# Performance work log

Hardware: AMD Instinct MI355X
Metric: run time of the kernel (lower is better)

The kernel has to match this reference:

```python
import jax, jax.numpy as jnp
import numpy as np

N_NODES = 100000
N_HEDGES = 20000
N_PAIRS = 1600000
D = 128


def setup_inputs() -> dict:
    key = jax.random.key(0)
    k1, k2, k3, k4, k5 = jax.random.split(key, 5)
    features = jax.random.normal(k1, (N_NODES, D), dtype=jnp.float32)
    W = jax.random.normal(k2, (D, D), dtype=jnp.float32) * (1.0 / np.sqrt(D))
    b = jax.random.normal(k3, (D,), dtype=jnp.float32) * 0.01
    node_idx = jax.random.randint(k4, (N_PAIRS,), 0, N_NODES, dtype=jnp.int32)
    hedge_idx = jax.random.randint(k5, (N_PAIRS,), 0, N_HEDGES, dtype=jnp.int32)
    return {"features": features, "W": W, "b": b,
            "node_idx": node_idx, "hedge_idx": hedge_idx, "n_hedges": N_HEDGES}


def reference(features, W, b, node_idx, hedge_idx, n_hedges):
    # features: [N, D]; (node_idx, hedge_idx): [E] incidence pairs
    N = features.shape[0]
    ones = jnp.ones(node_idx.shape, dtype=features.dtype)
    # node -> hyperedge mean (DGL copy_u + mean over 'in' etype)
    deg_e = jax.ops.segment_sum(ones, hedge_idx, num_segments=n_hedges)  # [He]
    h_edge = jax.ops.segment_sum(features[node_idx], hedge_idx, num_segments=n_hedges)
    h_edge = h_edge / jnp.maximum(deg_e, 1.0)[:, None]  # zero-degree edges -> 0
    # hyperedge -> node mean (copy_u + mean over 'contains' etype)
    deg_n = jax.ops.segment_sum(ones, node_idx, num_segments=N)  # [N]
    h_node = jax.ops.segment_sum(h_edge[hedge_idx], node_idx, num_segments=N)
    h_node = h_node / jnp.maximum(deg_n, 1.0)[:, None]
    # nn.Linear: x @ W.T + b
    return h_node @ W.T + b
```

## Files before the change

### kernel.cpp

```cpp
#include <hip/hip_runtime.h>

static constexpr int kD = 128;
static constexpr int kHedges = 20000;

static constexpr int kNCE = 157;
static constexpr int kCapCE = 11264;
static constexpr int kNCN = 196;
static constexpr int kCapCN = 9216;
static constexpr int kSliceE = 896;
static constexpr int kSliceN = 768;
static constexpr int kPmax = 3200;

__device__ __forceinline__ float u2f(unsigned u) { return __uint_as_float(u); }
__device__ __forceinline__ unsigned f2u(float f) { return __float_as_uint(f); }

__device__ __forceinline__ unsigned bfpack(float x, float y) {
  unsigned ux = f2u(x); ux = (ux + 0x7FFFu + ((ux >> 16) & 1u)) >> 16;
  unsigned uy = f2u(y); uy = (uy + 0x7FFFu + ((uy >> 16) & 1u)) & 0xFFFF0000u;
  return ux | uy;
}
__device__ __forceinline__ void bf8_acc(uint4 v, float* a) {
  a[0] += u2f(v.x << 16); a[1] += u2f(v.x & 0xFFFF0000u);
  a[2] += u2f(v.y << 16); a[3] += u2f(v.y & 0xFFFF0000u);
  a[4] += u2f(v.z << 16); a[5] += u2f(v.z & 0xFFFF0000u);
  a[6] += u2f(v.w << 16); a[7] += u2f(v.w & 0xFFFF0000u);
}

__global__ __launch_bounds__(256) void partition_coarse(
    const float* __restrict__ feat, unsigned* __restrict__ feat_bf, int n_feat,
    const int* __restrict__ node_idx, const int* __restrict__ hedge_idx,
    int n_pairs,
    int* __restrict__ gcnt_e, int* __restrict__ buf_e,
    int* __restrict__ gcnt_n, int* __restrict__ buf_n) {
  __shared__ unsigned lbuf_e[kPmax];
  __shared__ unsigned lbuf_n[kPmax];
  __shared__ int he[kNCE], se[kNCE];
  __shared__ int hn[kNCN], sn_[kNCN];
  __shared__ int wtot[4];
  const int tid = threadIdx.x;
  {
    const int n8 = n_feat >> 3;
    for (int t = blockIdx.x * 256 + tid; t < n8; t += gridDim.x * 256) {
      long long i = (long long)t * 8;
      const float4 v0 = *(const float4*)(feat + i);
      const float4 v1 = *(const float4*)(feat + i + 4);
      uint4 o;
      o.x = bfpack(v0.x, v0.y); o.y = bfpack(v0.z, v0.w);
      o.z = bfpack(v1.x, v1.y); o.w = bfpack(v1.z, v1.w);
      *(uint4*)(feat_bf + (i >> 1)) = o;
    }
  }
  const int per_block = (n_pairs + gridDim.x - 1) / gridDim.x;
  const int s = blockIdx.x * per_block;
  const int e = min(s + per_block, n_pairs);
  const int cnt = max(e - s, 0);
  for (int i = tid; i < kNCE; i += 256) he[i] = 0;
  for (int i = tid; i < kNCN; i += 256) hn[i] = 0;
  __syncthreads();
  for (int i = s + tid; i < e; i += 256) {
    atomicAdd(&he[hedge_idx[i] >> 7], 1);
    atomicAdd(&hn[node_idx[i] >> 9], 1);
  }
  __syncthreads();
  const int lane = tid & 63, wid = tid >> 6;
  {
    int v = (tid < kNCE) ? he[tid] : 0;
    int x = v;
#pragma unroll
    for (int d = 1; d < 64; d <<= 1) {
      int y = __shfl_up(x, d, 64);
      if (lane >= d) x += y;
    }
    if (lane == 63) wtot[wid] = x;
    __syncthreads();
    int add = 0;
    for (int w = 0; w < wid; ++w) add += wtot[w];
    if (tid < kNCE) {
      int lofs = x + add - v;
      int base = (v > 0) ? atomicAdd(&gcnt_e[tid], v) : 0;
      se[tid] = base - lofs;
      he[tid] = lofs;
    }
  }
  __syncthreads();
  {
    int v = (tid < kNCN) ? hn[tid] : 0;
    int x = v;
#pragma unroll
    for (int d = 1; d < 64; d <<= 1) {
      int y = __shfl_up(x, d, 64);
      if (lane >= d) x += y;
    }
    if (lane == 63) wtot[wid] = x;
    __syncthreads();
    int add = 0;
    for (int w = 0; w < wid; ++w) add += wtot[w];
    if (tid < kNCN) {
      int lofs = x + add - v;
      int base = (v > 0) ? atomicAdd(&gcnt_n[tid], v) : 0;
      sn_[tid] = base - lofs;
      hn[tid] = lofs;
    }
  }
  __syncthreads();
  for (int i = s + tid; i < e; i += 256) {
    const unsigned n = (unsigned)node_idx[i];
    const unsigned h = (unsigned)hedge_idx[i];
    const int be = (int)(h >> 7);
    const int p = atomicAdd(&he[be], 1);
    lbuf_e[p] = (n << 15) | h;
    const int bn = (int)(n >> 9);
    const int q = atomicAdd(&hn[bn], 1);
    lbuf_n[q] = (h << 17) | n;
  }
  __syncthreads();
  for (int i = tid; i < cnt; i += 256) {
    const unsigned v = lbuf_e[i];
    const int h = (int)(v & 0x7FFFu);
    const int n = (int)(v >> 15);
    const int b = h >> 7;
    const int pe = se[b] + i;
    if (pe < kCapCE) buf_e[(long long)b * kCapCE + pe] = (n << 7) | (h & 127);
  }
  for (int i = tid; i < cnt; i += 256) {
    const unsigned v = lbuf_n[i];
    const int n = (int)(v & 0x1FFFFu);
    const int h = (int)(v >> 17);
    const int b = n >> 9;
    const int pn = sn_[b] + i;
    if (pn < kCapCN) buf_n[(long long)b * kCapCN + pn] = (h << 9) | (n & 511);
  }
}

__global__ __launch_bounds__(512) void subsort_kernel(
    int* __restrict__ buf_e, const int* __restrict__ gcnt_e, int* __restrict__ seg_e,
    int* __restrict__ buf_n, const int* __restrict__ gcnt_n, int* __restrict__ seg_n) {
  __shared__ int sbuf[kCapCE];
  __shared__ int bins[513];
  __shared__ int cur[512];
  __shared__ int segs[513];
  __shared__ int wtot[8];
  const int tid = threadIdx.x;
  int nbins, shift, cnt; int* src; int* segout;
  if (blockIdx.x < kNCE) {
    int cb = blockIdx.x; nbins = 128; shift = 7;
    src = buf_e + (long long)cb * kCapCE;
    cnt = min(gcnt_e[cb], kCapCE);
    segout = seg_e + cb * 129;
  } else {
    int cb = blockIdx.x - kNCE; nbins = 512; shift = 9;
    src = buf_n + (long long)cb * kCapCN;
    cnt = min(gcnt_n[cb], kCapCN);
    segout = seg_n + cb * 513;
  }
  const int mask = nbins - 1;
  for (int i = tid; i < nbins; i += 512) bins[i] = 0;
  __syncthreads();
  for (int i = tid; i < cnt; i += 512) atomicAdd(&bins[src[i] & mask], 1);
  __syncthreads();
  const int lane = tid & 63, wid = tid >> 6;
  int v = (tid < nbins) ? bins[tid] : 0;
  int x = v;
#pragma unroll
  for (int d = 1; d < 64; d <<= 1) {
    int y = __shfl_up(x, d, 64);
    if (lane >= d) x += y;
  }
  if (lane == 63) wtot[wid] = x;
  __syncthreads();
  int add = 0;
  for (int w = 0; w < wid; ++w) add += wtot[w];
  if (tid < nbins) { segs[tid + 1] = x + add; cur[tid] = x + add - v; }
  if (tid == 0) segs[0] = 0;
  __syncthreads();
  for (int i = tid; i < cnt; i += 512) {
    int p = src[i];
    int r = atomicAdd(&cur[p & mask], 1);
    sbuf[r] = p >> shift;
  }
  __syncthreads();
  for (int i = tid; i < cnt; i += 512) src[i] = sbuf[i];
  for (int j = tid; j <= nbins; j += 512) segout[j] = segs[j];
}

__global__ __launch_bounds__(128) void gather_edge_v2(
    const unsigned* __restrict__ feat_bf, const int* __restrict__ buf_e,
    const int* __restrict__ seg_e, unsigned* __restrict__ h_edge, int n_hedges) {
  __shared__ int ebuf[kSliceE];
  __shared__ int segl[9];
  const int b = blockIdx.x;
  const int tid = threadIdx.x;
  const int h0 = b * 8;
  const int cb = h0 >> 7, j0 = h0 & 127;
  if (tid < 9) segl[tid] = seg_e[cb * 129 + j0 + tid];
  __syncthreads();
  const int sbase = segl[0];
  const int n_sl = min(segl[8] - sbase, kSliceE);
  const int* src = buf_e + (long long)cb * kCapCE + sbase;
  for (int i = tid; i < n_sl; i += 128) ebuf[i] = src[i];
  __syncthreads();
  const int g = tid >> 4, lane = tid & 15, cw = lane * 4;
  int gh = h0 + g;
  if (gh >= n_hedges) return;
  const int deg = segl[g + 1] - segl[g];
  const int s0 = min(segl[g] - sbase, n_sl);
  const int e0 = min(segl[g + 1] - sbase, n_sl);
  float a[8] = {}, a2[8] = {};
  int j = s0;
  for (; j + 7 < e0; j += 8) {
    uint4 v0 = *(const uint4*)(feat_bf + (long long)ebuf[j] * 64 + cw);
    uint4 v1 = *(const uint4*)(feat_bf + (long long)ebuf[j + 1] * 64 + cw);
    uint4 v2 = *(const uint4*)(feat_bf + (long long)ebuf[j + 2] * 64 + cw);
    uint4 v3 = *(const uint4*)(feat_bf + (long long)ebuf[j + 3] * 64 + cw);
    uint4 v4 = *(const uint4*)(feat_bf + (long long)ebuf[j + 4] * 64 + cw);
    uint4 v5 = *(const uint4*)(feat_bf + (long long)ebuf[j + 5] * 64 + cw);
    uint4 v6 = *(const uint4*)(feat_bf + (long long)ebuf[j + 6] * 64 + cw);
    uint4 v7 = *(const uint4*)(feat_bf + (long long)ebuf[j + 7] * 64 + cw);
    bf8_acc(v0, a); bf8_acc(v1, a2); bf8_acc(v2, a); bf8_acc(v3, a2);
    bf8_acc(v4, a); bf8_acc(v5, a2); bf8_acc(v6, a); bf8_acc(v7, a2);
  }
  for (; j < e0; ++j) {
    uint4 v = *(const uint4*)(feat_bf + (long long)ebuf[j] * 64 + cw);
    bf8_acc(v, a);
  }
#pragma unroll
  for (int t = 0; t < 8; ++t) a[t] += a2[t];
  float inv = 1.0f / fmaxf((float)deg, 1.0f);
  uint4 o;
  o.x = bfpack(a[0] * inv, a[1] * inv);
  o.y = bfpack(a[2] * inv, a[3] * inv);
  o.z = bfpack(a[4] * inv, a[5] * inv);
  o.w = bfpack(a[6] * inv, a[7] * inv);
  *(uint4*)(h_edge + (long long)gh * 64 + cw) = o;
}

static constexpr int kWRow = 68;
__global__ __launch_bounds__(256) void edge_linear_v4(
    unsigned* __restrict__ h_edge, const float* __restrict__ W, int n_rows) {
  __shared__ unsigned Wt2[kD * kWRow];
  __shared__ float hT[kD * 64];
  const int tid = threadIdx.x;
  const int row0 = blockIdx.x * 64;
  for (int i = tid; i < kD * 64; i += 256) {
    int k = i & 127, j = i >> 7;
    float c0 = W[(2 * j) * kD + k];
    float c1 = W[(2 * j + 1) * kD + k];
    Wt2[k * kWRow + j] = bfpack(c0, c1);
  }
  {
    const int r = tid & 63, o = tid >> 6;
    const uint4* hp = (const uint4*)(h_edge + (long long)(row0 + r) * 64 + o * 16);
#pragma unroll
    for (int q = 0; q < 4; ++q) {
      uint4 v = hp[q];
      int k0 = o * 32 + q * 8;
      hT[(k0 + 0) * 64 + r] = u2f(v.x << 16);
      hT[(k0 + 1) * 64 + r] = u2f(v.x & 0xFFFF0000u);
      hT[(k0 + 2) * 64 + r] = u2f(v.y << 16);
      hT[(k0 + 3) * 64 + r] = u2f(v.y & 0xFFFF0000u);
      hT[(k0 + 4) * 64 + r] = u2f(v.z << 16);
      hT[(k0 + 5) * 64 + r] = u2f(v.z & 0xFFFF0000u);
      hT[(k0 + 6) * 64 + r] = u2f(v.w << 16);
      hT[(k0 + 7) * 64 + r] = u2f(v.w & 0xFFFF0000u);
    }
  }
  __syncthreads();
  const int c8 = tid & 15;
  const int rg = tid >> 4;
  float4 acc[4][2] = {};
#pragma unroll 2
  for (int k = 0; k < kD; ++k) {
    const uint4 wp = *(const uint4*)(&Wt2[k * kWRow + c8 * 4]);
    const float4 h4 = *(const float4*)(&hT[k * 64 + rg * 4]);
    const float w0 = u2f(wp.x << 16), w1 = u2f(wp.x & 0xFFFF0000u);
    const float w2 = u2f(wp.y << 16), w3 = u2f(wp.y & 0xFFFF0000u);
    const float w4 = u2f(wp.z << 16), w5 = u2f(wp.z & 0xFFFF0000u);
    const float w6 = u2f(wp.w << 16), w7 = u2f(wp.w & 0xFFFF0000u);
    const float hh[4] = {h4.x, h4.y, h4.z, h4.w};
#pragma unroll
    for (int i = 0; i < 4; ++i) {
      acc[i][0].x = fmaf(hh[i], w0, acc[i][0].x);
      acc[i][0].y = fmaf(hh[i], w1, acc[i][0].y);
      acc[i][0].z = fmaf(hh[i], w2, acc[i][0].z);
      acc[i][0].w = fmaf(hh[i], w3, acc[i][0].w);
      acc[i][1].x = fmaf(hh[i], w4, acc[i][1].x);
      acc[i][1].y = fmaf(hh[i], w5, acc[i][1].y);
      acc[i][1].z = fmaf(hh[i], w6, acc[i][1].z);
      acc[i][1].w = fmaf(hh[i], w7, acc[i][1].w);
    }
  }
  long long rr = row0 + rg * 4;
#pragma unroll
  for (int i = 0; i < 4; ++i) {
    uint4 o;
    o.x = bfpack(acc[i][0].x, acc[i][0].y);
    o.y = bfpack(acc[i][0].z, acc[i][0].w);
    o.z = bfpack(acc[i][1].x, acc[i][1].y);
    o.w = bfpack(acc[i][1].z, acc[i][1].w);
    *(uint4*)(h_edge + (rr + i) * 64 + c8 * 4) = o;
  }
}

__global__ __launch_bounds__(128) void gather_node_v2(
    const unsigned* __restrict__ t_edge, const int* __restrict__ buf_n,
    const int* __restrict__ seg_n, const float* __restrict__ bias,
    float* __restrict__ out, int n_nodes) {
  __shared__ int ebuf[kSliceN];
  __shared__ int segl[33];
  const int b = blockIdx.x;
  const int tid = threadIdx.x;
  const int n0 = b * 32;
  const int cb = n0 >> 9, j0 = n0 & 511;
  if (tid < 33) segl[tid] = seg_n[cb * 513 + j0 + tid];
  __syncthreads();
  const int sbase = segl[0];
  const int n_sl = min(segl[32] - sbase, kSliceN);
  const int* src = buf_n + (long long)cb * kCapCN + sbase;
  for (int i = tid; i < n_sl; i += 128) ebuf[i] = src[i];
  __syncthreads();
  const int g = tid >> 4, lane = tid & 15, cw = lane * 4;
  const float4 b0 = *(const float4*)(bias + lane * 8);
  const float4 b1 = *(const float4*)(bias + lane * 8 + 4);
  for (int nl = g; nl < 32; nl += 8) {
    int gn = n0 + nl;
    if (gn >= n_nodes) continue;
    const int deg = segl[nl + 1] - segl[nl];
    const int s0 = min(segl[nl] - sbase, n_sl);
    const int e0 = min(segl[nl + 1] - sbase, n_sl);
    float a[8] = {}, a2[8] = {};
    int j = s0;
    for (; j + 7 < e0; j += 8) {
      uint4 v0 = *(const uint4*)(t_edge + (long long)ebuf[j] * 64 + cw);
      uint4 v1 = *(const uint4*)(t_edge + (long long)ebuf[j + 1] * 64 + cw);
      uint4 v2 = *(const uint4*)(t_edge + (long long)ebuf[j + 2] * 64 + cw);
      uint4 v3 = *(const uint4*)(t_edge + (long long)ebuf[j + 3] * 64 + cw);
      uint4 v4 = *(const uint4*)(t_edge + (long long)ebuf[j + 4] * 64 + cw);
      uint4 v5 = *(const uint4*)(t_edge + (long long)ebuf[j + 5] * 64 + cw);
      uint4 v6 = *(const uint4*)(t_edge + (long long)ebuf[j + 6] * 64 + cw);
      uint4 v7 = *(const uint4*)(t_edge + (long long)ebuf[j + 7] * 64 + cw);
      bf8_acc(v0, a); bf8_acc(v1, a2); bf8_acc(v2, a); bf8_acc(v3, a2);
      bf8_acc(v4, a); bf8_acc(v5, a2); bf8_acc(v6, a); bf8_acc(v7, a2);
    }
    for (; j < e0; ++j) {
      uint4 v = *(const uint4*)(t_edge + (long long)ebuf[j] * 64 + cw);
      bf8_acc(v, a);
    }
#pragma unroll
    for (int t = 0; t < 8; ++t) a[t] += a2[t];
    float inv = 1.0f / fmaxf((float)deg, 1.0f);
    float4 o0, o1;
    o0.x = fmaf(a[0], inv, b0.x); o0.y = fmaf(a[1], inv, b0.y);
    o0.z = fmaf(a[2], inv, b0.z); o0.w = fmaf(a[3], inv, b0.w);
    o1.x = fmaf(a[4], inv, b1.x); o1.y = fmaf(a[5], inv, b1.y);
    o1.z = fmaf(a[6], inv, b1.z); o1.w = fmaf(a[7], inv, b1.w);
    float* op = out + (long long)gn * kD + lane * 8;
    *(float4*)op = o0;
    *(float4*)(op + 4) = o1;
  }
}

extern "C" void kernel_launch(void* const* d_in, const int* in_sizes, int n_in,
                              void* d_out, int out_size, void* d_ws, size_t ws_size,
                              hipStream_t stream) {
  const float* feat      = (const float*)d_in[0];
  const float* W         = (const float*)d_in[1];
  const float* b         = (const float*)d_in[2];
  const int*   node_idx  = (const int*)d_in[3];
  const int*   hedge_idx = (const int*)d_in[4];

  const int n_pairs  = in_sizes[3];
  const int n_nodes  = in_sizes[0] / kD;
  const int n_hedges = kHedges;
  const int n_feat   = in_sizes[0];

  unsigned* feat_bf = (unsigned*)d_out;

  const int n_rows_pad = ((n_hedges + 63) / 64) * 64;
  unsigned* h_edge = (unsigned*)d_ws;
  int* buf_e = (int*)(h_edge + (size_t)n_rows_pad * 64);
  int* buf_n = buf_e + (size_t)kNCE * kCapCE;
  int* seg_e = buf_n + (size_t)kNCN * kCapCN;
  int* seg_n = seg_e + (size_t)kNCE * 129;
  int* gcnt_e = seg_n + (size_t)kNCN * 513;
  int* gcnt_n = gcnt_e + kNCE;

  hipMemsetAsync(gcnt_e, 0, (size_t)(kNCE + kNCN) * sizeof(int), stream);

  int pgrid = (n_pairs + kPmax - 1) / kPmax;
  if (pgrid < 512) pgrid = 512;

  partition_coarse<<<pgrid, 256, 0, stream>>>(
      feat, feat_bf, n_feat,
      node_idx, hedge_idx, n_pairs, gcnt_e, buf_e, gcnt_n, buf_n);

  subsort_kernel<<<kNCE + kNCN, 512, 0, stream>>>(
      buf_e, gcnt_e, seg_e, buf_n, gcnt_n, seg_n);

  gather_edge_v2<<<(n_hedges + 7) / 8, 128, 0, stream>>>(
      feat_bf, buf_e, seg_e, h_edge, n_hedges);

  edge_linear_v4<<<n_rows_pad / 64, 256, 0, stream>>>(h_edge, W, n_rows_pad);

  gather_node_v2<<<(n_nodes + 31) / 32, 128, 0, stream>>>(
      h_edge, buf_n, seg_n, b, (float*)d_out, n_nodes);
}
```

Measured before the change: 277.2 us.

## Split gather kernels across eight feature-column slices per block group

Both gather kernels now launch eight blocks per node/hyperedge group, each block handling a 16-column slice with one 4-byte bf16-pair load per thread instead of a 16-byte load. This raises parallelism and occupancy, with 256-thread blocks and more hyperedges per block. The cost is that every slice block reloads the index list into shared memory, and the gathered loads are narrower and less coalesced. The edge slice buffer grows to 3072 entries, and the index loads and edge output stores become nontemporal.

```diff
diff --git a/kernel.cpp b/kernel.cpp
--- a/kernel.cpp
+++ b/kernel.cpp
@@ -7,7 +7,7 @@
 static constexpr int kCapCE = 11264;
 static constexpr int kNCN = 196;
 static constexpr int kCapCN = 9216;
-static constexpr int kSliceE = 896;
+static constexpr int kSliceE3 = 3072;
 static constexpr int kSliceN = 768;
 static constexpr int kPmax = 3200;
 
@@ -18,12 +18,6 @@
   unsigned ux = f2u(x); ux = (ux + 0x7FFFu + ((ux >> 16) & 1u)) >> 16;
   unsigned uy = f2u(y); uy = (uy + 0x7FFFu + ((uy >> 16) & 1u)) & 0xFFFF0000u;
   return ux | uy;
-}
-__device__ __forceinline__ void bf8_acc(uint4 v, float* a) {
-  a[0] += u2f(v.x << 16); a[1] += u2f(v.x & 0xFFFF0000u);
-  a[2] += u2f(v.y << 16); a[3] += u2f(v.y & 0xFFFF0000u);
-  a[4] += u2f(v.z << 16); a[5] += u2f(v.z & 0xFFFF0000u);
-  a[6] += u2f(v.w << 16); a[7] += u2f(v.w & 0xFFFF0000u);
 }
 
 __global__ __launch_bounds__(256) void partition_coarse(
@@ -183,55 +177,60 @@
   for (int j = tid; j <= nbins; j += 512) segout[j] = segs[j];
 }
 
-__global__ __launch_bounds__(128) void gather_edge_v2(
+__global__ __launch_bounds__(256) void gather_edge_v3(
     const unsigned* __restrict__ feat_bf, const int* __restrict__ buf_e,
     const int* __restrict__ seg_e, unsigned* __restrict__ h_edge, int n_hedges) {
-  __shared__ int ebuf[kSliceE];
-  __shared__ int segl[9];
-  const int b = blockIdx.x;
-  const int tid = threadIdx.x;
-  const int h0 = b * 8;
+  __shared__ int ebuf[kSliceE3];
+  __shared__ int segl[33];
+  const int bid = blockIdx.x;
+  const int slice = bid & 7;
+  const int hb = bid >> 3;
+  const int tid = threadIdx.x;
+  const int h0 = hb * 32;
   const int cb = h0 >> 7, j0 = h0 & 127;
-  if (tid < 9) segl[tid] = seg_e[cb * 129 + j0 + tid];
+  if (tid < 33) segl[tid] = seg_e[cb * 129 + j0 + tid];
   __syncthreads();
   const int sbase = segl[0];
-  const int n_sl = min(segl[8] - sbase, kSliceE);
+  const int n_sl = min(segl[32] - sbase, kSliceE3);
   const int* src = buf_e + (long long)cb * kCapCE + sbase;
-  for (int i = tid; i < n_sl; i += 128) ebuf[i] = src[i];
-  __syncthreads();
-  const int g = tid >> 4, lane = tid & 15, cw = lane * 4;
-  int gh = h0 + g;
+  for (int i = tid; i < n_sl; i += 256) ebuf[i] = __builtin_nontemporal_load(&src[i]);
+  __syncthreads();
+  const int g = tid >> 3, lane = tid & 7;
+  const int gh = h0 + g;
   if (gh >= n_hedges) return;
+  const int w = slice * 8 + lane;
+  const unsigned* fw = feat_bf + w;
   const int deg = segl[g + 1] - segl[g];
   const int s0 = min(segl[g] - sbase, n_sl);
   const int e0 = min(segl[g + 1] - sbase, n_sl);
-  float a[8] = {}, a2[8] = {};
+  float a0 = 0.f, a1 = 0.f, c0 = 0.f, c1 = 0.f;
   int j = s0;
   for (; j + 7 < e0; j += 8) {
-    uint4 v0 = *(const uint4*)(feat_bf + (long long)ebuf[j] * 64 + cw);
-    uint4 v1 = *(const uint4*)(feat_bf + (long long)ebuf[j + 1] * 64 + cw);
-    uint4 v2 = *(const uint4*)(feat_bf + (long long)ebuf[j + 2] * 64 + cw);
-    uint4 v3 = *(const uint4*)(feat_bf + (long long)ebuf[j + 3] * 64 + cw);
-    uint4 v4 = *(const uint4*)(feat_bf + (long long)ebuf[j + 4] * 64 + cw);
-    uint4 v5 = *(const uint4*)(feat_bf + (long long)ebuf[j + 5] * 64 + cw);
-    uint4 v6 = *(const uint4*)(feat_bf + (long long)ebuf[j + 6] * 64 + cw);
-    uint4 v7 = *(const uint4*)(feat_bf + (long long)ebuf[j + 7] * 64 + cw);
-    bf8_acc(v0, a); bf8_acc(v1, a2); bf8_acc(v2, a); bf8_acc(v3, a2);
-    bf8_acc(v4, a); bf8_acc(v5, a2); bf8_acc(v6, a); bf8_acc(v7, a2);
+    unsigned u0 = fw[(unsigned)ebuf[j] * 64u];
+    unsigned u1 = fw[(unsigned)ebuf[j + 1] * 64u];
+    unsigned u2 = fw[(unsigned)ebuf[j + 2] * 64u];
+    unsigned u3 = fw[(unsigned)ebuf[j + 3] * 64u];
+    unsigned u4 = fw[(unsigned)ebuf[j + 4] * 64u];
+    unsigned u5 = fw[(unsigned)ebuf[j + 5] * 64u];
+    unsigned u6 = fw[(unsigned)ebuf[j + 6] * 64u];
+    unsigned u7 = fw[(unsigned)ebuf[j + 7] * 64u];
+    a0 += u2f(u0 << 16); a1 += u2f(u0 & 0xFFFF0000u);
+    c0 += u2f(u1 << 16); c1 += u2f(u1 & 0xFFFF0000u);
+    a0 += u2f(u2 << 16); a1 += u2f(u2 & 0xFFFF0000u);
+    c0 += u2f(u3 << 16); c1 += u2f(u3 & 0xFFFF0000u);
+    a0 += u2f(u4 << 16); a1 += u2f(u4 & 0xFFFF0000u);
+    c0 += u2f(u5 << 16); c1 += u2f(u5 & 0xFFFF0000u);
+    a0 += u2f(u6 << 16); a1 += u2f(u6 & 0xFFFF0000u);
+    c0 += u2f(u7 << 16); c1 += u2f(u7 & 0xFFFF0000u);
   }
   for (; j < e0; ++j) {
-    uint4 v = *(const uint4*)(feat_bf + (long long)ebuf[j] * 64 + cw);
-    bf8_acc(v, a);
-  }
-#pragma unroll
-  for (int t = 0; t < 8; ++t) a[t] += a2[t];
-  float inv = 1.0f / fmaxf((float)deg, 1.0f);
-  uint4 o;
-  o.x = bfpack(a[0] * inv, a[1] * inv);
-  o.y = bfpack(a[2] * inv, a[3] * inv);
-  o.z = bfpack(a[4] * inv, a[5] * inv);
-  o.w = bfpack(a[6] * inv, a[7] * inv);
-  *(uint4*)(h_edge + (long long)gh * 64 + cw) = o;
+    unsigned u = fw[(unsigned)ebuf[j] * 64u];
+    a0 += u2f(u << 16); a1 += u2f(u & 0xFFFF0000u);
+  }
+  a0 += c0; a1 += c1;
+  const float inv = 1.0f / fmaxf((float)deg, 1.0f);
+  __builtin_nontemporal_store(bfpack(a0 * inv, a1 * inv),
+                              &h_edge[(unsigned)gh * 64u + w]);
 }
 
 static constexpr int kWRow = 68;
@@ -301,62 +300,56 @@
   }
 }
 
-__global__ __launch_bounds__(128) void gather_node_v2(
+__global__ __launch_bounds__(256) void gather_node_v3(
     const unsigned* __restrict__ t_edge, const int* __restrict__ buf_n,
     const int* __restrict__ seg_n, const float* __restrict__ bias,
     float* __restrict__ out, int n_nodes) {
   __shared__ int ebuf[kSliceN];
   __shared__ int segl[33];
-  const int b = blockIdx.x;
-  const int tid = threadIdx.x;
-  const int n0 = b * 32;
+  const int bid = blockIdx.x;
+  const int slice = bid & 7;
+  const int nb = bid >> 3;
+  const int tid = threadIdx.x;
+  const int n0 = nb * 32;
   const int cb = n0 >> 9, j0 = n0 & 511;
   if (tid < 33) segl[tid] = seg_n[cb * 513 + j0 + tid];
   __syncthreads();
   const int sbase = segl[0];
   const int n_sl = min(segl[32] - sbase, kSliceN);
   const int* src = buf_n + (long long)cb * kCapCN + sbase;
-  for (int i = tid; i < n_sl; i += 128) ebuf[i] = src[i];
-  __syncthreads();
-  const int g = tid >> 4, lane = tid & 15, cw = lane * 4;
-  const float4 b0 = *(const float4*)(bias + lane * 8);
-  const float4 b1 = *(const float4*)(bias + lane * 8 + 4);
-  for (int nl = g; nl < 32; nl += 8) {
-    int gn = n0 + nl;
-    if (gn >= n_nodes) continue;
-    const int deg = segl[nl + 1] - segl[nl];
-    const int s0 = min(segl[nl] - sbase, n_sl);
-    const int e0 = min(segl[nl + 1] - sbase, n_sl);
-    float a[8] = {}, a2[8] = {};
-    int j = s0;
-    for (; j + 7 < e0; j += 8) {
-      uint4 v0 = *(const uint4*)(t_edge + (long long)ebuf[j] * 64 + cw);
-      uint4 v1 = *(const uint4*)(t_edge + (long long)ebuf[j + 1] * 64 + cw);
-      uint4 v2 = *(const uint4*)(t_edge + (long long)ebuf[j + 2] * 64 + cw);
-      uint4 v3 = *(const uint4*)(t_edge + (long long)ebuf[j + 3] * 64 + cw);
-      uint4 v4 = *(const uint4*)(t_edge + (long long)ebuf[j + 4] * 64 + cw);
-      uint4 v5 = *(const uint4*)(t_edge + (long long)ebuf[j + 5] * 64 + cw);
-      uint4 v6 = *(const uint4*)(t_edge + (long long)ebuf[j + 6] * 64 + cw);
-      uint4 v7 = *(const uint4*)(t_edge + (long long)ebuf[j + 7] * 64 + cw);
-      bf8_acc(v0, a); bf8_acc(v1, a2); bf8_acc(v2, a); bf8_acc(v3, a2);
-      bf8_acc(v4, a); bf8_acc(v5, a2); bf8_acc(v6, a); bf8_acc(v7, a2);
-    }
-    for (; j < e0; ++j) {
-      uint4 v = *(const uint4*)(t_edge + (long long)ebuf[j] * 64 + cw);
-      bf8_acc(v, a);
-    }
-#pragma unroll
-    for (int t = 0; t < 8; ++t) a[t] += a2[t];
-    float inv = 1.0f / fmaxf((float)deg, 1.0f);
-    float4 o0, o1;
-    o0.x = fmaf(a[0], inv, b0.x); o0.y = fmaf(a[1], inv, b0.y);
-    o0.z = fmaf(a[2], inv, b0.z); o0.w = fmaf(a[3], inv, b0.w);
-    o1.x = fmaf(a[4], inv, b1.x); o1.y = fmaf(a[5], inv, b1.y);
-    o1.z = fmaf(a[6], inv, b1.z); o1.w = fmaf(a[7], inv, b1.w);
-    float* op = out + (long long)gn * kD + lane * 8;
-    *(float4*)op = o0;
-    *(float4*)(op + 4) = o1;
-  }
+  for (int i = tid; i < n_sl; i += 256) ebuf[i] = __builtin_nontemporal_load(&src[i]);
+  __syncthreads();
+  const int g = tid >> 3, lane = tid & 7;
+  const int gn = n0 + g;
+  if (gn >= n_nodes) return;
+  const int w = slice * 8 + lane;
+  const unsigned* tw = t_edge + w;
+  const float2 bb = *(const float2*)(bias + 2 * w);
+  const int deg = segl[g + 1] - segl[g];
+  const int s0 = min(segl[g] - sbase, n_sl);
+  const int e0 = min(segl[g + 1] - sbase, n_sl);
+  float a0 = 0.f, a1 = 0.f, c0 = 0.f, c1 = 0.f;
+  int j = s0;
+  for (; j + 3 < e0; j += 4) {
+    unsigned u0 = tw[(unsigned)ebuf[j] * 64u];
+    unsigned u1 = tw[(unsigned)ebuf[j + 1] * 64u];
+    unsigned u2 = tw[(unsigned)ebuf[j + 2] * 64u];
+    unsigned u3 = tw[(unsigned)ebuf[j + 3] * 64u];
+    a0 += u2f(u0 << 16); a1 += u2f(u0 & 0xFFFF0000u);
+    c0 += u2f(u1 << 16); c1 += u2f(u1 & 0xFFFF0000u);
+    a0 += u2f(u2 << 16); a1 += u2f(u2 & 0xFFFF0000u);
+    c0 += u2f(u3 << 16); c1 += u2f(u3 & 0xFFFF0000u);
+  }
+  for (; j < e0; ++j) {
+    unsigned u = tw[(unsigned)ebuf[j] * 64u];
+    a0 += u2f(u << 16); a1 += u2f(u & 0xFFFF0000u);
+  }
+  a0 += c0; a1 += c1;
+  const float inv = 1.0f / fmaxf((float)deg, 1.0f);
+  float2 o;
+  o.x = fmaf(a0, inv, bb.x);
+  o.y = fmaf(a1, inv, bb.y);
+  *(float2*)(out + (long long)gn * kD + 2 * w) = o;
 }
 
 extern "C" void kernel_launch(void* const* d_in, const int* in_sizes, int n_in,
@@ -396,11 +389,11 @@
   subsort_kernel<<<kNCE + kNCN, 512, 0, stream>>>(
       buf_e, gcnt_e, seg_e, buf_n, gcnt_n, seg_n);
 
-  gather_edge_v2<<<(n_hedges + 7) / 8, 128, 0, stream>>>(
+  gather_edge_v3<<<8 * ((n_hedges + 31) / 32), 256, 0, stream>>>(
       feat_bf, buf_e, seg_e, h_edge, n_hedges);
 
   edge_linear_v4<<<n_rows_pad / 64, 256, 0, stream>>>(h_edge, W, n_rows_pad);
 
-  gather_node_v2<<<(n_nodes + 31) / 32, 128, 0, stream>>>(
+  gather_node_v3<<<8 * ((n_nodes + 31) / 32), 256, 0, stream>>>(
       h_edge, buf_n, seg_n, b, (float*)d_out, n_nodes);
 }
```

New measurement: 443.9 us. +60.2%, slower.
